# Optimization experiments

Hardware: AMD Instinct MI355X
Metric: run time of the kernel (lower is better)

The kernel has to match this reference:

```python
import jax, jax.numpy as jnp
import numpy as np

MAXHD, MAXV, MINA, MAXA, DT = 100.0, 40.0, -6.0, 4.0, 0.1
UNITS, IN_DIM = 20, 12


def setup_inputs() -> dict:
    key = jax.random.key(0)
    ks = jax.random.split(key, 12)
    nveh, nt = 8192, 1000
    lead_fol_inputs = jax.random.uniform(ks[0], (nveh, nt, 12), dtype=jnp.float32) * 50.0
    init_state = jax.random.uniform(ks[1], (nveh, 2), dtype=jnp.float32) * 20.0
    h0 = jnp.zeros((nveh, UNITS), jnp.float32)
    c0 = jnp.zeros((nveh, UNITS), jnp.float32)
    s = 0.1
    return {
        'lead_fol_inputs': lead_fol_inputs,
        'init_state': init_state,
        'h0': h0,
        'c0': c0,
        'lstm_kernel': jax.random.normal(ks[2], (IN_DIM, 4 * UNITS), jnp.float32) * s,
        'lstm_rec_kernel': jax.random.normal(ks[3], (UNITS, 4 * UNITS), jnp.float32) * s,
        'lstm_bias': jnp.zeros((4 * UNITS,), jnp.float32),
        'd2_w': jax.random.normal(ks[4], (UNITS, 10), jnp.float32) * s,
        'd2_b': jnp.zeros((10,), jnp.float32),
        'lc_w': jax.random.normal(ks[5], (10, 3), jnp.float32) * s,
        'lc_b': jnp.zeros((3,), jnp.float32),
        'd1_w': jax.random.normal(ks[6], (10, 1), jnp.float32) * s,
        'd1_b': jnp.zeros((1,), jnp.float32),
    }


def reference(lead_fol_inputs, init_state, h0, c0, lstm_kernel, lstm_rec_kernel,
              lstm_bias, d2_w, d2_b, lc_w, lc_b, d1_w, d1_b):
    # lead_fol_inputs: (nveh, nt, 12) -> scan over time axis
    xs = jnp.transpose(lead_fol_inputs, (1, 0, 2))  # (nt, nveh, 12)
    pos0 = init_state[:, 0]
    spd0 = init_state[:, 1]

    def step(carry, inp):
        pos, spd, h, c = carry
        lead_hd = (inp[:, :3] - pos[:, None]) / MAXHD
        fol_hd = (pos[:, None] - inp[:, 3:6]) / MAXHD
        spds = inp[:, 6:] / MAXV
        cur = jnp.concatenate([lead_hd, fol_hd, spds], axis=1)  # (nveh, 12)
        cur = jnp.where(jnp.isnan(cur), jnp.ones_like(cur), cur)
        # Keras LSTMCell: gate order i, f, g, o
        z = cur @ lstm_kernel + h @ lstm_rec_kernel + lstm_bias
        i, f, g, o = jnp.split(z, 4, axis=1)
        c = jax.nn.sigmoid(f) * c + jax.nn.sigmoid(i) * jnp.tanh(g)
        h = jax.nn.sigmoid(o) * jnp.tanh(c)
        x = jax.nn.relu(h @ d2_w + d2_b)          # dense2, (nveh, 10)
        lc = x @ lc_w + lc_b                      # lc_actions, (nveh, 3)
        acc_raw = (x @ d1_w + d1_b)[:, 0]         # dense1, (nveh,)
        acc = (MAXA - MINA) * acc_raw + MINA
        pos = pos + DT * spd
        spd = spd + DT * acc
        return (pos, spd, h, c), (pos, lc)

    (pos_f, spd_f, h_f, c_f), (pos_seq, lc_seq) = jax.lax.scan(
        step, (pos0, spd0, h0, c0), xs)
    pos_outputs = jnp.transpose(pos_seq, (1, 0))        # (nveh, nt)
    lc_outputs = jnp.transpose(lc_seq, (1, 0, 2))       # (nveh, nt, 3)
    curspeed = spd_f[:, None]                            # (nveh, 1)
    return pos_outputs, lc_outputs, curspeed, (h_f, c_f)
```

## Files before the change

### kernel.cpp

```cpp
#include <hip/hip_runtime.h>


typedef __attribute__((ext_vector_type(8))) short short8;
typedef __attribute__((ext_vector_type(4))) short short4v;
typedef __attribute__((ext_vector_type(4))) float float4v;
typedef __attribute__((ext_vector_type(2))) float float2v;

__device__ __forceinline__ short f2b(float f) {
    unsigned u = __float_as_uint(f);
    u += 0x7fffu + ((u >> 16) & 1u);
    return (short)(u >> 16);
}

__device__ __forceinline__ float fast_exp2(float x) {
#if __has_builtin(__builtin_amdgcn_exp2f)
    return __builtin_amdgcn_exp2f(x);
#else
    return exp2f(x);
#endif
}
__device__ __forceinline__ float fast_rcp(float x) {
#if __has_builtin(__builtin_amdgcn_rcpf)
    return __builtin_amdgcn_rcpf(x);
#else
    return 1.0f / x;
#endif
}

#define L2E 1.44269504088896340736f

__global__ void __launch_bounds__(128) rnncf_kernel(
    const float* __restrict__ inp,
    const float* __restrict__ init_state,
    const float* __restrict__ h0g,
    const float* __restrict__ c0g,
    const float* __restrict__ Wk,
    const float* __restrict__ Wr,
    const float* __restrict__ bz_g,
    const float* __restrict__ W2,
    const float* __restrict__ b2_g,
    const float* __restrict__ Wlc,
    const float* __restrict__ blc,
    const float* __restrict__ Wd1,
    const float* __restrict__ bd1,
    float* __restrict__ out)
{
    __shared__ short h_lds[2][16 * 36];

    const int tid = threadIdx.x;
    const int wv  = tid >> 6;
    const int l   = tid & 63;
    const int q   = l >> 4;
    const int col = l & 15;
    const int v0  = (blockIdx.x * 2 + wv) * 16;

    short* hl  = h_lds[wv];
    char*  hl8 = (char*)hl;

    float* out_pos = out;
    float* out_lc  = out + 8192000;
    float* out_spd = out + 32768000;
    float* out_h   = out + 32776192;
    float* out_c   = out + 32940032;

    const int g  = col & 3;
    const int cu = col >> 2;
    const float sg_a = (g == 2) ? 2.0f * L2E : -L2E;

    short8  w1t[5];
    float4v bz1[5];
#pragma unroll
    for (int p = 0; p < 5; ++p) {
        const int ua = (p < 4) ? (4 * cu + p) : (16 + cu);
        const int n  = g * 20 + ua;
#pragma unroll
        for (int j = 0; j < 8; ++j) {
            int k = 8 * q + j;
            float wvl = (k < 12) ? Wk[k * 80 + n] : Wr[(k - 12) * 80 + n];
            w1t[p][j] = f2b(wvl * sg_a);
        }
        const int ud = (p < 4) ? (4 * q + p) : (16 + q);
#pragma unroll
        for (int r = 0; r < 4; ++r) {
            float sr = (r == 2) ? 2.0f * L2E : -L2E;
            bz1[p][r] = sr * bz_g[r * 20 + ud];
        }
    }

    short8 w2t;
#pragma unroll
    for (int j = 0; j < 8; ++j) {
        int k = 8 * q + j;
        float v = (col < 10 && k < 20) ? W2[k * 10 + col] : 0.0f;
        w2t[j] = f2b(v);
    }
    float4v bx;
#pragma unroll
    for (int r = 0; r < 4; ++r) { int n = 4 * q + r; bx[r] = (n < 10) ? b2_g[n] : 0.0f; }

    float wd3[4][4];
#pragma unroll
    for (int r = 0; r < 4; ++r) {
        int f = 4 * q + r;
#pragma unroll
        for (int o = 0; o < 4; ++o)
            wd3[r][o] = (f < 10) ? ((o < 3) ? Wlc[f * 3 + o] : Wd1[f]) : 0.0f;
    }
    const float lc_bias = (q < 3) ? blc[q] : 0.0f;
    const float bd1v    = bd1[0];

    const int base = col * 72;
    const int o1 = (q == 0) ? 0 : (q == 1) ? 16 : (q == 2) ? 32 : 24;
    const int o2 = (q == 0) ? 8 : (q == 1) ? 24 : (q == 2) ? 8  : 32;
    const int o3 = (q == 2) ? 16 : 0;
    const int a1 = base + o1, a2 = base + o2, a3 = base + o3;
    const int awr = base + 8 * q;

    float c_st[5], h_keep[5];
#pragma unroll
    for (int p = 0; p < 5; ++p) {
        const int ud = (p < 4) ? (4 * q + p) : (16 + q);
        c_st[p] = c0g[(size_t)(v0 + col) * 20 + ud];
        h_keep[p] = 0.0f;
    }
    for (int i = l; i < 16 * 36; i += 64) hl[i] = 0;
    {
        short4v h0w;
#pragma unroll
        for (int p = 0; p < 4; ++p)
            h0w[p] = f2b(h0g[(size_t)(v0 + col) * 20 + 4 * q + p]);
        *(short4v*)(hl8 + awr) = h0w;
        hl[col * 36 + 16 + q] = f2b(h0g[(size_t)(v0 + col) * 20 + 16 + q]);
    }

    float2v ps = *(const float2v*)(init_state + (size_t)(v0 + col) * 2);
    float pos = ps[0], spd = ps[1];

    const float* ipbase = inp + (size_t)(v0 + col) * 12000;
    float4v inA = {0, 0, 0, 0}, inB = {0, 0, 0, 0}, inC = {0, 0, 0, 0};
    if (q == 0)      { inA = *(const float4v*)(ipbase); inB = *(const float4v*)(ipbase + 4); }
    else if (q == 1) { inC = *(const float4v*)(ipbase + 8); }

    short4v r1 = *(const short4v*)(hl8 + a1);
    short4v r2 = *(const short4v*)(hl8 + a2);
    short4v r3 = *(const short4v*)(hl8 + a3);

#pragma unroll 2
    for (int t = 0; t < 1000; ++t) {
        short8 bfrag;
        if (q == 0) {
            float pp = pos * 0.01f;
            bfrag[0] = f2b(__builtin_fmaf(inA[0],  0.01f, -pp));
            bfrag[1] = f2b(__builtin_fmaf(inA[1],  0.01f, -pp));
            bfrag[2] = f2b(__builtin_fmaf(inA[2],  0.01f, -pp));
            bfrag[3] = f2b(__builtin_fmaf(inA[3], -0.01f,  pp));
            bfrag[4] = f2b(__builtin_fmaf(inB[0], -0.01f,  pp));
            bfrag[5] = f2b(__builtin_fmaf(inB[1], -0.01f,  pp));
            bfrag[6] = f2b(inB[2] * 0.025f);
            bfrag[7] = f2b(inB[3] * 0.025f);
        } else if (q == 1) {
            bfrag[0] = f2b(inC[0] * 0.025f);
            bfrag[1] = f2b(inC[1] * 0.025f);
            bfrag[2] = f2b(inC[2] * 0.025f);
            bfrag[3] = f2b(inC[3] * 0.025f);
            bfrag[4] = r3[0]; bfrag[5] = r3[1]; bfrag[6] = r3[2]; bfrag[7] = r3[3];
        } else if (q == 2) {
            bfrag[0] = r2[0]; bfrag[1] = r2[1]; bfrag[2] = r2[2]; bfrag[3] = r2[3];
            bfrag[4] = r3[0]; bfrag[5] = r3[1]; bfrag[6] = r3[2]; bfrag[7] = r3[3];
        } else {
            bfrag[0] = r1[0]; bfrag[1] = r1[1]; bfrag[2] = r1[2]; bfrag[3] = r1[3];
            bfrag[4] = r2[0]; bfrag[5] = r2[1]; bfrag[6] = r2[2]; bfrag[7] = r2[3];
        }

        float4v z[5];
#pragma unroll
        for (int p = 0; p < 5; ++p)
            z[p] = __builtin_amdgcn_mfma_f32_16x16x32_bf16(w1t[p], bfrag, bz1[p], 0, 0, 0);

        {
            int tn = (t < 999) ? t + 1 : 999;
            const float* ipn = ipbase + tn * 12;
            if (q == 0)      { inA = *(const float4v*)(ipn); inB = *(const float4v*)(ipn + 4); }
            else if (q == 1) { inC = *(const float4v*)(ipn + 8); }
        }

        short4v hw;
        short h16 = 0;
#pragma unroll
        for (int p = 0; p < 5; ++p) {
            float zi = fminf(z[p][0], 29.f);
            float zf = fminf(z[p][1], 29.f);
            float zg = fminf(z[p][2], 58.f);
            float zo = fminf(z[p][3], 29.f);
            float eA = fast_exp2(zi);
            float eB = fast_exp2(zf);
            float eC = fast_exp2(zg);
            float eD = fast_exp2(zo);
            float pA = 1.0f + eA, pB = 1.0f + eB, pC = eC + 1.0f, mC = eC - 1.0f;
            float t1 = pA * pC;
            float R  = fast_rcp(t1 * pB);
            float cn = (c_st[p] * t1 + mC * pB) * R;
            c_st[p] = cn;
            float ec = fminf(cn * (2.0f * L2E), 58.f);
            float eE = fast_exp2(ec);
            float h  = (eE - 1.0f) * fast_rcp((1.0f + eD) * (eE + 1.0f));
            h_keep[p] = h;
            short hb = f2b(h);
            if (p < 4) hw[p] = hb; else h16 = hb;
        }
        *(short4v*)(hl8 + awr) = hw;
        hl[col * 36 + 16 + q] = h16;

        r1 = *(const short4v*)(hl8 + a1);
        r2 = *(const short4v*)(hl8 + a2);
        r3 = *(const short4v*)(hl8 + a3);

        short8 hfrag;
        hfrag[0] = r1[0]; hfrag[1] = r1[1]; hfrag[2] = r1[2]; hfrag[3] = r1[3];
        hfrag[4] = r2[0]; hfrag[5] = r2[1]; hfrag[6] = r2[2]; hfrag[7] = r2[3];
        float4v x4 = __builtin_amdgcn_mfma_f32_16x16x32_bf16(w2t, hfrag, bx, 0, 0, 0);
        float xr[4];
#pragma unroll
        for (int r = 0; r < 4; ++r) xr[r] = fmaxf(x4[r], 0.0f);

        float pd[4];
#pragma unroll
        for (int o = 0; o < 4; ++o) {
            float s = xr[0] * wd3[0][o];
            s = __builtin_fmaf(xr[1], wd3[1][o], s);
            s = __builtin_fmaf(xr[2], wd3[2][o], s);
            s = __builtin_fmaf(xr[3], wd3[3][o], s);
            s += __shfl_xor(s, 16);
            s += __shfl_xor(s, 32);
            pd[o] = s;
        }
        float lcv = pd[0];
        lcv = (q == 1) ? pd[1] : lcv;
        lcv = (q == 2) ? pd[2] : lcv;
        if (q < 3)
            out_lc[(size_t)(v0 + col) * 3000 + t * 3 + q] = lcv + lc_bias;

        pos = __builtin_fmaf(0.1f, spd, pos);
        if (q == 0) out_pos[(size_t)(v0 + col) * 1000 + t] = pos;
        float acc = __builtin_fmaf(10.0f, pd[3] + bd1v, -6.0f);
        spd = __builtin_fmaf(0.1f, acc, spd);
    }

    if (q == 0) out_spd[v0 + col] = spd;
#pragma unroll
    for (int p = 0; p < 5; ++p) {
        const int ud = (p < 4) ? (4 * q + p) : (16 + q);
        out_h[(size_t)(v0 + col) * 20 + ud] = h_keep[p];
        out_c[(size_t)(v0 + col) * 20 + ud] = c_st[p];
    }
}

extern "C" void kernel_launch(void* const* d_in, const int* in_sizes, int n_in,
                              void* d_out, int out_size, void* d_ws, size_t ws_size,
                              hipStream_t stream) {
    rnncf_kernel<<<256, 128, 0, stream>>>(
        (const float*)d_in[0],  (const float*)d_in[1],  (const float*)d_in[2],
        (const float*)d_in[3],  (const float*)d_in[4],  (const float*)d_in[5],
        (const float*)d_in[6],  (const float*)d_in[7],  (const float*)d_in[8],
        (const float*)d_in[9],  (const float*)d_in[10], (const float*)d_in[11],
        (const float*)d_in[12], (float*)d_out);
}
```

Measured before the change: 1.338 ms.

## Skew dense head one step behind LSTM and use MFMA for output projection

Restructures the time loop so the dense2/lc/dense1 head for step t-1 runs at the start of step t, overlapping it with the LSTM gate MFMAs instead of serialising after the h write. The final projection, previously per-lane FMAs plus cross-lane shuffles, becomes a single f16 MFMA with biases folded into its accumulator. Input prefetch is also deepened to two steps ahead. The head now uses f16 for the relu outputs and weights, which adds rounding error, and the loop needs an epilogue to handle the last step.

After: 1.398 ms. +4.5%, slower.

```diff
diff --git a/kernel.cpp b/kernel.cpp
--- a/kernel.cpp
+++ b/kernel.cpp
@@ -5,6 +5,7 @@
 typedef __attribute__((ext_vector_type(4))) short short4v;
 typedef __attribute__((ext_vector_type(4))) float float4v;
 typedef __attribute__((ext_vector_type(2))) float float2v;
+typedef __attribute__((ext_vector_type(4))) _Float16 half4;
 
 __device__ __forceinline__ short f2b(float f) {
     unsigned u = __float_as_uint(f);
@@ -28,6 +29,12 @@
 }
 
 #define L2E 1.44269504088896340736f
+
+#if __has_builtin(__builtin_amdgcn_mfma_f32_16x16x16f16)
+#define HAVE_MFMA_D 1
+#else
+#define HAVE_MFMA_D 0
+#endif
 
 __global__ void __launch_bounds__(128) rnncf_kernel(
     const float* __restrict__ inp,
@@ -98,6 +105,23 @@
 #pragma unroll
     for (int r = 0; r < 4; ++r) { int n = 4 * q + r; bx[r] = (n < 10) ? b2_g[n] : 0.0f; }
 
+#if HAVE_MFMA_D
+    half4 a2;
+#pragma unroll
+    for (int j = 0; j < 4; ++j) {
+        int k = 4 * q + j;
+        float wv2 = 0.0f;
+        if (k < 10) {
+            if (col < 3)       wv2 = Wlc[k * 3 + col];
+            else if (col == 3) wv2 = Wd1[k];
+        }
+        a2[j] = (_Float16)wv2;
+    }
+    float4v c2;
+#pragma unroll
+    for (int r = 0; r < 4; ++r)
+        c2[r] = (q == 0) ? ((r < 3) ? blc[r] : bd1[0]) : 0.0f;
+#else
     float wd3[4][4];
 #pragma unroll
     for (int r = 0; r < 4; ++r) {
@@ -106,14 +130,14 @@
         for (int o = 0; o < 4; ++o)
             wd3[r][o] = (f < 10) ? ((o < 3) ? Wlc[f * 3 + o] : Wd1[f]) : 0.0f;
     }
-    const float lc_bias = (q < 3) ? blc[q] : 0.0f;
-    const float bd1v    = bd1[0];
+    const float blc0 = blc[0], blc1 = blc[1], blc2 = blc[2], bd1v = bd1[0];
+#endif
 
     const int base = col * 72;
     const int o1 = (q == 0) ? 0 : (q == 1) ? 16 : (q == 2) ? 32 : 24;
     const int o2 = (q == 0) ? 8 : (q == 1) ? 24 : (q == 2) ? 8  : 32;
     const int o3 = (q == 2) ? 16 : 0;
-    const int a1 = base + o1, a2 = base + o2, a3 = base + o3;
+    const int a1 = base + o1, a2a = base + o2, a3 = base + o3;
     const int awr = base + 8 * q;
 
     float c_st[5], h_keep[5];
@@ -138,11 +162,17 @@
 
     const float* ipbase = inp + (size_t)(v0 + col) * 12000;
     float4v inA = {0, 0, 0, 0}, inB = {0, 0, 0, 0}, inC = {0, 0, 0, 0};
-    if (q == 0)      { inA = *(const float4v*)(ipbase); inB = *(const float4v*)(ipbase + 4); }
-    else if (q == 1) { inC = *(const float4v*)(ipbase + 8); }
+    float4v nA  = {0, 0, 0, 0}, nB  = {0, 0, 0, 0}, nC  = {0, 0, 0, 0};
+    if (q == 0) {
+        inA = *(const float4v*)(ipbase);      inB = *(const float4v*)(ipbase + 4);
+        nA  = *(const float4v*)(ipbase + 12); nB  = *(const float4v*)(ipbase + 16);
+    } else if (q == 1) {
+        inC = *(const float4v*)(ipbase + 8);
+        nC  = *(const float4v*)(ipbase + 20);
+    }
 
     short4v r1 = *(const short4v*)(hl8 + a1);
-    short4v r2 = *(const short4v*)(hl8 + a2);
+    short4v r2 = *(const short4v*)(hl8 + a2a);
     short4v r3 = *(const short4v*)(hl8 + a3);
 
 #pragma unroll 2
@@ -177,12 +207,64 @@
         for (int p = 0; p < 5; ++p)
             z[p] = __builtin_amdgcn_mfma_f32_16x16x32_bf16(w1t[p], bfrag, bz1[p], 0, 0, 0);
 
+        inA = nA; inB = nB; inC = nC;
         {
-            int tn = (t < 999) ? t + 1 : 999;
+            int tn = t + 2; if (tn > 999) tn = 999;
             const float* ipn = ipbase + tn * 12;
-            if (q == 0)      { inA = *(const float4v*)(ipn); inB = *(const float4v*)(ipn + 4); }
-            else if (q == 1) { inC = *(const float4v*)(ipn + 8); }
-        }
+            if (q == 0)      { nA = *(const float4v*)(ipn); nB = *(const float4v*)(ipn + 4); }
+            else if (q == 1) { nC = *(const float4v*)(ipn + 8); }
+        }
+
+        {
+            short8 hfrag;
+            hfrag[0] = r1[0]; hfrag[1] = r1[1]; hfrag[2] = r1[2]; hfrag[3] = r1[3];
+            hfrag[4] = r2[0]; hfrag[5] = r2[1]; hfrag[6] = r2[2]; hfrag[7] = r2[3];
+            float4v x4 = __builtin_amdgcn_mfma_f32_16x16x32_bf16(w2t, hfrag, bx, 0, 0, 0);
+#if HAVE_MFMA_D
+            half4 b2;
+#pragma unroll
+            for (int r = 0; r < 4; ++r) b2[r] = (_Float16)fmaxf(x4[r], 0.0f);
+            float4v pd = __builtin_amdgcn_mfma_f32_16x16x16f16(a2, b2, c2, 0, 0, 0);
+            if (t) {
+                if (q == 0) {
+                    size_t lci = (size_t)(v0 + col) * 3000 + (size_t)(t - 1) * 3;
+                    out_lc[lci + 0] = pd[0];
+                    out_lc[lci + 1] = pd[1];
+                    out_lc[lci + 2] = pd[2];
+                }
+                float acc = __builtin_fmaf(10.0f, pd[3], -6.0f);
+                spd = __builtin_fmaf(0.1f, acc, spd);
+            }
+#else
+            float xr[4];
+#pragma unroll
+            for (int r = 0; r < 4; ++r) xr[r] = fmaxf(x4[r], 0.0f);
+            float pd[4];
+#pragma unroll
+            for (int o = 0; o < 4; ++o) {
+                float s = xr[0] * wd3[0][o];
+                s = __builtin_fmaf(xr[1], wd3[1][o], s);
+                s = __builtin_fmaf(xr[2], wd3[2][o], s);
+                s = __builtin_fmaf(xr[3], wd3[3][o], s);
+                s += __shfl_xor(s, 16);
+                s += __shfl_xor(s, 32);
+                pd[o] = s;
+            }
+            if (t) {
+                if (q == 0) {
+                    size_t lci = (size_t)(v0 + col) * 3000 + (size_t)(t - 1) * 3;
+                    out_lc[lci + 0] = pd[0] + blc0;
+                    out_lc[lci + 1] = pd[1] + blc1;
+                    out_lc[lci + 2] = pd[2] + blc2;
+                }
+                float acc = __builtin_fmaf(10.0f, pd[3] + bd1v, -6.0f);
+                spd = __builtin_fmaf(0.1f, acc, spd);
+            }
+#endif
+        }
+
+        pos = __builtin_fmaf(0.1f, spd, pos);
+        if (q == 0) out_pos[(size_t)(v0 + col) * 1000 + t] = pos;
 
         short4v hw;
         short h16 = 0;
@@ -212,17 +294,33 @@
         hl[col * 36 + 16 + q] = h16;
 
         r1 = *(const short4v*)(hl8 + a1);
-        r2 = *(const short4v*)(hl8 + a2);
+        r2 = *(const short4v*)(hl8 + a2a);
         r3 = *(const short4v*)(hl8 + a3);
-
+    }
+
+    {
         short8 hfrag;
         hfrag[0] = r1[0]; hfrag[1] = r1[1]; hfrag[2] = r1[2]; hfrag[3] = r1[3];
         hfrag[4] = r2[0]; hfrag[5] = r2[1]; hfrag[6] = r2[2]; hfrag[7] = r2[3];
         float4v x4 = __builtin_amdgcn_mfma_f32_16x16x32_bf16(w2t, hfrag, bx, 0, 0, 0);
+#if HAVE_MFMA_D
+        half4 b2;
+#pragma unroll
+        for (int r = 0; r < 4; ++r) b2[r] = (_Float16)fmaxf(x4[r], 0.0f);
+        float4v pd = __builtin_amdgcn_mfma_f32_16x16x16f16(a2, b2, c2, 0, 0, 0);
+        if (q == 0) {
+            size_t lci = (size_t)(v0 + col) * 3000 + 999 * 3;
+            out_lc[lci + 0] = pd[0];
+            out_lc[lci + 1] = pd[1];
+            out_lc[lci + 2] = pd[2];
+            float acc = __builtin_fmaf(10.0f, pd[3], -6.0f);
+            spd = __builtin_fmaf(0.1f, acc, spd);
+            out_spd[v0 + col] = spd;
+        }
+#else
         float xr[4];
 #pragma unroll
         for (int r = 0; r < 4; ++r) xr[r] = fmaxf(x4[r], 0.0f);
-
         float pd[4];
 #pragma unroll
         for (int o = 0; o < 4; ++o) {
@@ -234,19 +332,18 @@
             s += __shfl_xor(s, 32);
             pd[o] = s;
         }
-        float lcv = pd[0];
-        lcv = (q == 1) ? pd[1] : lcv;
-        lcv = (q == 2) ? pd[2] : lcv;
-        if (q < 3)
-            out_lc[(size_t)(v0 + col) * 3000 + t * 3 + q] = lcv + lc_bias;
-
-        pos = __builtin_fmaf(0.1f, spd, pos);
-        if (q == 0) out_pos[(size_t)(v0 + col) * 1000 + t] = pos;
-        float acc = __builtin_fmaf(10.0f, pd[3] + bd1v, -6.0f);
-        spd = __builtin_fmaf(0.1f, acc, spd);
-    }
-
-    if (q == 0) out_spd[v0 + col] = spd;
+        if (q == 0) {
+            size_t lci = (size_t)(v0 + col) * 3000 + 999 * 3;
+            out_lc[lci + 0] = pd[0] + blc0;
+            out_lc[lci + 1] = pd[1] + blc1;
+            out_lc[lci + 2] = pd[2] + blc2;
+            float acc = __builtin_fmaf(10.0f, pd[3] + bd1v, -6.0f);
+            spd = __builtin_fmaf(0.1f, acc, spd);
+            out_spd[v0 + col] = spd;
+        }
+#endif
+    }
+
 #pragma unroll
     for (int p = 0; p < 5; ++p) {
         const int ud = (p < 4) ? (4 * q + p) : (16 + q);
```

## Interleave two vehicle groups per wavefront to hide recurrent latency

Applied to the files above, without the earlier changes.

Each wavefront now processes two independent 16-vehicle groups in lockstep instead of one, with a 64-thread block per 32 vehicles. Independent MFMA and transcendental chains from the two groups can be interleaved, hiding the serial per-timestep latency of the LSTM recurrence. The cost is half as many wavefronts overall (256 waves on a 256-CU part), higher register pressure, and the loop unroll dropping to 1.

Measured after the change: 2.181 ms. 1.63x slower.

```diff
diff --git a/kernel.cpp b/kernel.cpp
--- a/kernel.cpp
+++ b/kernel.cpp
@@ -29,7 +29,7 @@
 
 #define L2E 1.44269504088896340736f
 
-__global__ void __launch_bounds__(128) rnncf_kernel(
+__global__ void __launch_bounds__(64, 1) rnncf_kernel(
     const float* __restrict__ inp,
     const float* __restrict__ init_state,
     const float* __restrict__ h0g,
@@ -47,15 +47,12 @@
 {
     __shared__ short h_lds[2][16 * 36];
 
-    const int tid = threadIdx.x;
-    const int wv  = tid >> 6;
-    const int l   = tid & 63;
+    const int l   = threadIdx.x & 63;
     const int q   = l >> 4;
     const int col = l & 15;
-    const int v0  = (blockIdx.x * 2 + wv) * 16;
-
-    short* hl  = h_lds[wv];
-    char*  hl8 = (char*)hl;
+    const int vb  = blockIdx.x * 32;
+
+    char* hl8 = (char*)h_lds;
 
     float* out_pos = out;
     float* out_lc  = out + 8192000;
@@ -63,16 +60,16 @@
     float* out_h   = out + 32776192;
     float* out_c   = out + 32940032;
 
-    const int g  = col & 3;
+    const int gi = col & 3;
     const int cu = col >> 2;
-    const float sg_a = (g == 2) ? 2.0f * L2E : -L2E;
+    const float sg_a = (gi == 2) ? 2.0f * L2E : -L2E;
 
     short8  w1t[5];
     float4v bz1[5];
 #pragma unroll
     for (int p = 0; p < 5; ++p) {
         const int ua = (p < 4) ? (4 * cu + p) : (16 + cu);
-        const int n  = g * 20 + ua;
+        const int n  = gi * 20 + ua;
 #pragma unroll
         for (int j = 0; j < 8; ++j) {
             int k = 8 * q + j;
@@ -113,152 +110,204 @@
     const int o1 = (q == 0) ? 0 : (q == 1) ? 16 : (q == 2) ? 32 : 24;
     const int o2 = (q == 0) ? 8 : (q == 1) ? 24 : (q == 2) ? 8  : 32;
     const int o3 = (q == 2) ? 16 : 0;
-    const int a1 = base + o1, a2 = base + o2, a3 = base + o3;
+    const int a1 = base + o1, a2a = base + o2, a3 = base + o3;
     const int awr = base + 8 * q;
 
-    float c_st[5], h_keep[5];
-#pragma unroll
-    for (int p = 0; p < 5; ++p) {
-        const int ud = (p < 4) ? (4 * q + p) : (16 + q);
-        c_st[p] = c0g[(size_t)(v0 + col) * 20 + ud];
-        h_keep[p] = 0.0f;
-    }
-    for (int i = l; i < 16 * 36; i += 64) hl[i] = 0;
-    {
+    float c_st[2][5], h_keep[2][5];
+    float pos[2], spd[2];
+#pragma unroll
+    for (int grp = 0; grp < 2; ++grp) {
+        const int v = vb + grp * 16 + col;
+#pragma unroll
+        for (int p = 0; p < 5; ++p) {
+            const int ud = (p < 4) ? (4 * q + p) : (16 + q);
+            c_st[grp][p] = c0g[(size_t)v * 20 + ud];
+            h_keep[grp][p] = 0.0f;
+        }
+    }
+    for (int i = l; i < 2 * 16 * 36; i += 64) ((short*)h_lds)[i] = 0;
+#pragma unroll
+    for (int grp = 0; grp < 2; ++grp) {
+        const int v = vb + grp * 16 + col;
         short4v h0w;
 #pragma unroll
         for (int p = 0; p < 4; ++p)
-            h0w[p] = f2b(h0g[(size_t)(v0 + col) * 20 + 4 * q + p]);
-        *(short4v*)(hl8 + awr) = h0w;
-        hl[col * 36 + 16 + q] = f2b(h0g[(size_t)(v0 + col) * 20 + 16 + q]);
-    }
-
-    float2v ps = *(const float2v*)(init_state + (size_t)(v0 + col) * 2);
-    float pos = ps[0], spd = ps[1];
-
-    const float* ipbase = inp + (size_t)(v0 + col) * 12000;
-    float4v inA = {0, 0, 0, 0}, inB = {0, 0, 0, 0}, inC = {0, 0, 0, 0};
-    if (q == 0)      { inA = *(const float4v*)(ipbase); inB = *(const float4v*)(ipbase + 4); }
-    else if (q == 1) { inC = *(const float4v*)(ipbase + 8); }
-
-    short4v r1 = *(const short4v*)(hl8 + a1);
-    short4v r2 = *(const short4v*)(hl8 + a2);
-    short4v r3 = *(const short4v*)(hl8 + a3);
-
-#pragma unroll 2
+            h0w[p] = f2b(h0g[(size_t)v * 20 + 4 * q + p]);
+        *(short4v*)(hl8 + grp * 1152 + awr) = h0w;
+        h_lds[grp][col * 36 + 16 + q] = f2b(h0g[(size_t)v * 20 + 16 + q]);
+        float2v ps = *(const float2v*)(init_state + (size_t)v * 2);
+        pos[grp] = ps[0]; spd[grp] = ps[1];
+    }
+
+    const float* ip0 = inp + (size_t)(vb + col) * 12000;
+    const float* ip1 = inp + (size_t)(vb + 16 + col) * 12000;
+    float4v inA[2], inB[2], inC[2];
+#pragma unroll
+    for (int grp = 0; grp < 2; ++grp) { inA[grp] = float4v{0,0,0,0}; inB[grp] = float4v{0,0,0,0}; inC[grp] = float4v{0,0,0,0}; }
+    if (q == 0) {
+        inA[0] = *(const float4v*)(ip0); inB[0] = *(const float4v*)(ip0 + 4);
+        inA[1] = *(const float4v*)(ip1); inB[1] = *(const float4v*)(ip1 + 4);
+    } else if (q == 1) {
+        inC[0] = *(const float4v*)(ip0 + 8);
+        inC[1] = *(const float4v*)(ip1 + 8);
+    }
+
+    short4v r1[2], r2[2], r3[2];
+#pragma unroll
+    for (int grp = 0; grp < 2; ++grp) {
+        r1[grp] = *(const short4v*)(hl8 + grp * 1152 + a1);
+        r2[grp] = *(const short4v*)(hl8 + grp * 1152 + a2a);
+        r3[grp] = *(const short4v*)(hl8 + grp * 1152 + a3);
+    }
+
+#pragma unroll 1
     for (int t = 0; t < 1000; ++t) {
-        short8 bfrag;
-        if (q == 0) {
-            float pp = pos * 0.01f;
-            bfrag[0] = f2b(__builtin_fmaf(inA[0],  0.01f, -pp));
-            bfrag[1] = f2b(__builtin_fmaf(inA[1],  0.01f, -pp));
-            bfrag[2] = f2b(__builtin_fmaf(inA[2],  0.01f, -pp));
-            bfrag[3] = f2b(__builtin_fmaf(inA[3], -0.01f,  pp));
-            bfrag[4] = f2b(__builtin_fmaf(inB[0], -0.01f,  pp));
-            bfrag[5] = f2b(__builtin_fmaf(inB[1], -0.01f,  pp));
-            bfrag[6] = f2b(inB[2] * 0.025f);
-            bfrag[7] = f2b(inB[3] * 0.025f);
-        } else if (q == 1) {
-            bfrag[0] = f2b(inC[0] * 0.025f);
-            bfrag[1] = f2b(inC[1] * 0.025f);
-            bfrag[2] = f2b(inC[2] * 0.025f);
-            bfrag[3] = f2b(inC[3] * 0.025f);
-            bfrag[4] = r3[0]; bfrag[5] = r3[1]; bfrag[6] = r3[2]; bfrag[7] = r3[3];
-        } else if (q == 2) {
-            bfrag[0] = r2[0]; bfrag[1] = r2[1]; bfrag[2] = r2[2]; bfrag[3] = r2[3];
-            bfrag[4] = r3[0]; bfrag[5] = r3[1]; bfrag[6] = r3[2]; bfrag[7] = r3[3];
-        } else {
-            bfrag[0] = r1[0]; bfrag[1] = r1[1]; bfrag[2] = r1[2]; bfrag[3] = r1[3];
-            bfrag[4] = r2[0]; bfrag[5] = r2[1]; bfrag[6] = r2[2]; bfrag[7] = r2[3];
-        }
-
-        float4v z[5];
-#pragma unroll
-        for (int p = 0; p < 5; ++p)
-            z[p] = __builtin_amdgcn_mfma_f32_16x16x32_bf16(w1t[p], bfrag, bz1[p], 0, 0, 0);
+        short8 bfrag[2];
+#pragma unroll
+        for (int grp = 0; grp < 2; ++grp) {
+            if (q == 0) {
+                float pp = pos[grp] * 0.01f;
+                bfrag[grp][0] = f2b(__builtin_fmaf(inA[grp][0],  0.01f, -pp));
+                bfrag[grp][1] = f2b(__builtin_fmaf(inA[grp][1],  0.01f, -pp));
+                bfrag[grp][2] = f2b(__builtin_fmaf(inA[grp][2],  0.01f, -pp));
+                bfrag[grp][3] = f2b(__builtin_fmaf(inA[grp][3], -0.01f,  pp));
+                bfrag[grp][4] = f2b(__builtin_fmaf(inB[grp][0], -0.01f,  pp));
+                bfrag[grp][5] = f2b(__builtin_fmaf(inB[grp][1], -0.01f,  pp));
+                bfrag[grp][6] = f2b(inB[grp][2] * 0.025f);
+                bfrag[grp][7] = f2b(inB[grp][3] * 0.025f);
+            } else if (q == 1) {
+                bfrag[grp][0] = f2b(inC[grp][0] * 0.025f);
+                bfrag[grp][1] = f2b(inC[grp][1] * 0.025f);
+                bfrag[grp][2] = f2b(inC[grp][2] * 0.025f);
+                bfrag[grp][3] = f2b(inC[grp][3] * 0.025f);
+                bfrag[grp][4] = r3[grp][0]; bfrag[grp][5] = r3[grp][1];
+                bfrag[grp][6] = r3[grp][2]; bfrag[grp][7] = r3[grp][3];
+            } else if (q == 2) {
+                bfrag[grp][0] = r2[grp][0]; bfrag[grp][1] = r2[grp][1];
+                bfrag[grp][2] = r2[grp][2]; bfrag[grp][3] = r2[grp][3];
+                bfrag[grp][4] = r3[grp][0]; bfrag[grp][5] = r3[grp][1];
+                bfrag[grp][6] = r3[grp][2]; bfrag[grp][7] = r3[grp][3];
+            } else {
+                bfrag[grp][0] = r1[grp][0]; bfrag[grp][1] = r1[grp][1];
+                bfrag[grp][2] = r1[grp][2]; bfrag[grp][3] = r1[grp][3];
+                bfrag[grp][4] = r2[grp][0]; bfrag[grp][5] = r2[grp][1];
+                bfrag[grp][6] = r2[grp][2]; bfrag[grp][7] = r2[grp][3];
+            }
+        }
+
+        float4v z[2][5];
+#pragma unroll
+        for (int grp = 0; grp < 2; ++grp)
+#pragma unroll
+            for (int p = 0; p < 5; ++p)
+                z[grp][p] = __builtin_amdgcn_mfma_f32_16x16x32_bf16(w1t[p], bfrag[grp], bz1[p], 0, 0, 0);
 
         {
             int tn = (t < 999) ? t + 1 : 999;
-            const float* ipn = ipbase + tn * 12;
-            if (q == 0)      { inA = *(const float4v*)(ipn); inB = *(const float4v*)(ipn + 4); }
-            else if (q == 1) { inC = *(const float4v*)(ipn + 8); }
-        }
-
-        short4v hw;
-        short h16 = 0;
+            const float* p0 = ip0 + tn * 12;
+            const float* p1 = ip1 + tn * 12;
+            if (q == 0) {
+                inA[0] = *(const float4v*)(p0); inB[0] = *(const float4v*)(p0 + 4);
+                inA[1] = *(const float4v*)(p1); inB[1] = *(const float4v*)(p1 + 4);
+            } else if (q == 1) {
+                inC[0] = *(const float4v*)(p0 + 8);
+                inC[1] = *(const float4v*)(p1 + 8);
+            }
+        }
+
+#pragma unroll
+        for (int grp = 0; grp < 2; ++grp) {
+            short4v hw;
+            short h16 = 0;
+#pragma unroll
+            for (int p = 0; p < 5; ++p) {
+                float zi = fminf(z[grp][p][0], 29.f);
+                float zf = fminf(z[grp][p][1], 29.f);
+                float zg = fminf(z[grp][p][2], 58.f);
+                float zo = fminf(z[grp][p][3], 29.f);
+                float eA = fast_exp2(zi);
+                float eB = fast_exp2(zf);
+                float eC = fast_exp2(zg);
+                float eD = fast_exp2(zo);
+                float pA = 1.0f + eA, pB = 1.0f + eB, pC = eC + 1.0f, mC = eC - 1.0f;
+                float t1 = pA * pC;
+                float R  = fast_rcp(t1 * pB);
+                float cn = (c_st[grp][p] * t1 + mC * pB) * R;
+                c_st[grp][p] = cn;
+                float ec = fminf(cn * (2.0f * L2E), 58.f);
+                float eE = fast_exp2(ec);
+                float h  = (eE - 1.0f) * fast_rcp((1.0f + eD) * (eE + 1.0f));
+                h_keep[grp][p] = h;
+                short hb = f2b(h);
+                if (p < 4) hw[p] = hb; else h16 = hb;
+            }
+            *(short4v*)(hl8 + grp * 1152 + awr) = hw;
+            h_lds[grp][col * 36 + 16 + q] = h16;
+        }
+
+#pragma unroll
+        for (int grp = 0; grp < 2; ++grp) {
+            r1[grp] = *(const short4v*)(hl8 + grp * 1152 + a1);
+            r2[grp] = *(const short4v*)(hl8 + grp * 1152 + a2a);
+            r3[grp] = *(const short4v*)(hl8 + grp * 1152 + a3);
+        }
+
+#pragma unroll
+        for (int grp = 0; grp < 2; ++grp) {
+            short8 hfrag;
+            hfrag[0] = r1[grp][0]; hfrag[1] = r1[grp][1];
+            hfrag[2] = r1[grp][2]; hfrag[3] = r1[grp][3];
+            hfrag[4] = r2[grp][0]; hfrag[5] = r2[grp][1];
+            hfrag[6] = r2[grp][2]; hfrag[7] = r2[grp][3];
+            float4v x4 = __builtin_amdgcn_mfma_f32_16x16x32_bf16(w2t, hfrag, bx, 0, 0, 0);
+            float xr[4];
+#pragma unroll
+            for (int r = 0; r < 4; ++r) xr[r] = fmaxf(x4[r], 0.0f);
+
+            float pd[4];
+#pragma unroll
+            for (int o = 0; o < 4; ++o) {
+                float s = xr[0] * wd3[0][o];
+                s = __builtin_fmaf(xr[1], wd3[1][o], s);
+                s = __builtin_fmaf(xr[2], wd3[2][o], s);
+                s = __builtin_fmaf(xr[3], wd3[3][o], s);
+                s += __shfl_xor(s, 16);
+                s += __shfl_xor(s, 32);
+                pd[o] = s;
+            }
+            float lcv = pd[0];
+            lcv = (q == 1) ? pd[1] : lcv;
+            lcv = (q == 2) ? pd[2] : lcv;
+            if (q < 3)
+                out_lc[(size_t)(vb + grp * 16 + col) * 3000 + t * 3 + q] = lcv + lc_bias;
+
+            pos[grp] = __builtin_fmaf(0.1f, spd[grp], pos[grp]);
+            if (q == 0) out_pos[(size_t)(vb + grp * 16 + col) * 1000 + t] = pos[grp];
+            float acc = __builtin_fmaf(10.0f, pd[3] + bd1v, -6.0f);
+            spd[grp] = __builtin_fmaf(0.1f, acc, spd[grp]);
+        }
+    }
+
+    if (q == 0) {
+        out_spd[vb + col]      = spd[0];
+        out_spd[vb + 16 + col] = spd[1];
+    }
+#pragma unroll
+    for (int grp = 0; grp < 2; ++grp) {
+        const int v = vb + grp * 16 + col;
 #pragma unroll
         for (int p = 0; p < 5; ++p) {
-            float zi = fminf(z[p][0], 29.f);
-            float zf = fminf(z[p][1], 29.f);
-            float zg = fminf(z[p][2], 58.f);
-            float zo = fminf(z[p][3], 29.f);
-            float eA = fast_exp2(zi);
-            float eB = fast_exp2(zf);
-            float eC = fast_exp2(zg);
-            float eD = fast_exp2(zo);
-            float pA = 1.0f + eA, pB = 1.0f + eB, pC = eC + 1.0f, mC = eC - 1.0f;
-            float t1 = pA * pC;
-            float R  = fast_rcp(t1 * pB);
-            float cn = (c_st[p] * t1 + mC * pB) * R;
-            c_st[p] = cn;
-            float ec = fminf(cn * (2.0f * L2E), 58.f);
-            float eE = fast_exp2(ec);
-            float h  = (eE - 1.0f) * fast_rcp((1.0f + eD) * (eE + 1.0f));
-            h_keep[p] = h;
-            short hb = f2b(h);
-            if (p < 4) hw[p] = hb; else h16 = hb;
-        }
-        *(short4v*)(hl8 + awr) = hw;
-        hl[col * 36 + 16 + q] = h16;
-
-        r1 = *(const short4v*)(hl8 + a1);
-        r2 = *(const short4v*)(hl8 + a2);
-        r3 = *(const short4v*)(hl8 + a3);
-
-        short8 hfrag;
-        hfrag[0] = r1[0]; hfrag[1] = r1[1]; hfrag[2] = r1[2]; hfrag[3] = r1[3];
-        hfrag[4] = r2[0]; hfrag[5] = r2[1]; hfrag[6] = r2[2]; hfrag[7] = r2[3];
-        float4v x4 = __builtin_amdgcn_mfma_f32_16x16x32_bf16(w2t, hfrag, bx, 0, 0, 0);
-        float xr[4];
-#pragma unroll
-        for (int r = 0; r < 4; ++r) xr[r] = fmaxf(x4[r], 0.0f);
-
-        float pd[4];
-#pragma unroll
-        for (int o = 0; o < 4; ++o) {
-            float s = xr[0] * wd3[0][o];
-            s = __builtin_fmaf(xr[1], wd3[1][o], s);
-            s = __builtin_fmaf(xr[2], wd3[2][o], s);
-            s = __builtin_fmaf(xr[3], wd3[3][o], s);
-            s += __shfl_xor(s, 16);
-            s += __shfl_xor(s, 32);
-            pd[o] = s;
-        }
-        float lcv = pd[0];
-        lcv = (q == 1) ? pd[1] : lcv;
-        lcv = (q == 2) ? pd[2] : lcv;
-        if (q < 3)
-            out_lc[(size_t)(v0 + col) * 3000 + t * 3 + q] = lcv + lc_bias;
-
-        pos = __builtin_fmaf(0.1f, spd, pos);
-        if (q == 0) out_pos[(size_t)(v0 + col) * 1000 + t] = pos;
-        float acc = __builtin_fmaf(10.0f, pd[3] + bd1v, -6.0f);
-        spd = __builtin_fmaf(0.1f, acc, spd);
-    }
-
-    if (q == 0) out_spd[v0 + col] = spd;
-#pragma unroll
-    for (int p = 0; p < 5; ++p) {
-        const int ud = (p < 4) ? (4 * q + p) : (16 + q);
-        out_h[(size_t)(v0 + col) * 20 + ud] = h_keep[p];
-        out_c[(size_t)(v0 + col) * 20 + ud] = c_st[p];
+            const int ud = (p < 4) ? (4 * q + p) : (16 + q);
+            out_h[(size_t)v * 20 + ud] = h_keep[grp][p];
+            out_c[(size_t)v * 20 + ud] = c_st[grp][p];
+        }
     }
 }
 
 extern "C" void kernel_launch(void* const* d_in, const int* in_sizes, int n_in,
                               void* d_out, int out_size, void* d_ws, size_t ws_size,
                               hipStream_t stream) {
-    rnncf_kernel<<<256, 128, 0, stream>>>(
+    rnncf_kernel<<<256, 64, 0, stream>>>(
         (const float*)d_in[0],  (const float*)d_in[1],  (const float*)d_in[2],
         (const float*)d_in[3],  (const float*)d_in[4],  (const float*)d_in[5],
         (const float*)d_in[6],  (const float*)d_in[7],  (const float*)d_in[8],
```
